# Optimization experiments

Hardware: AMD Instinct MI355X
Metric: run time of the kernel (lower is better)

## Reference

```python
import jax, jax.numpy as jnp
import numpy as np

N = 100000
E = 3200000
D = 128


def setup_inputs() -> dict:
    key = jax.random.key(0)
    k1, k2, k3, k4 = jax.random.split(key, 4)
    x = jax.random.normal(k1, (N, D), dtype=jnp.float32)
    edge_index = jax.random.randint(k2, (2, E), 0, N, dtype=jnp.int64)
    W1 = jax.random.normal(k3, (D, 16), dtype=jnp.float32) * (1.0 / np.sqrt(D))
    b1 = jnp.zeros((16,), dtype=jnp.float32)
    W2 = jax.random.normal(k4, (16, 2), dtype=jnp.float32) * (1.0 / np.sqrt(16))
    b2 = jnp.zeros((2,), dtype=jnp.float32)
    return {"x": x, "edge_index": edge_index, "W1": W1, "b1": b1, "W2": W2, "b2": b2}


def _gcn_conv(h, src, dst, norm, W, b):
    # transform first (out_dim <= in_dim), then normalized scatter-add aggregation
    h = h @ W                                   # [N, out]
    msg = h[src] * norm[:, None]                # [E+N, out] gathered messages
    agg = jax.ops.segment_sum(msg, dst, num_segments=N)
    return agg + b


def reference(x, edge_index, W1, b1, W2, b2):
    loops = jnp.arange(N, dtype=edge_index.dtype)
    src = jnp.concatenate([edge_index[0], loops])   # row (message source)
    dst = jnp.concatenate([edge_index[1], loops])   # col (aggregation target)
    # symmetric GCN normalization: deg over dst, norm = d^-1/2[src] * d^-1/2[dst]
    deg = jax.ops.segment_sum(jnp.ones_like(src, dtype=x.dtype), dst, num_segments=N)
    dinv = jnp.where(deg > 0, jax.lax.rsqrt(deg), 0.0)
    norm = dinv[src] * dinv[dst]

    h = _gcn_conv(x, src, dst, norm, W1, b1)
    h = jax.nn.relu(h)
    h = _gcn_conv(h, src, dst, norm, W2, b2)
    return jax.nn.log_softmax(h, axis=1)
```

## Files before the change

### kernel.cpp

```cpp
#include <hip/hip_runtime.h>
#include <hip/hip_fp16.h>
#include <math.h>

#define N_NODES 100000
#define N_EDGES 3200000
#define D_IN    128
#define H1      16

#define PSH     8
#define NPB     200
#define NB      500
#define CAP     9936
#define PBLK    512
#define CHUNK   6250
#define ELS_CAP 13760
#define NLINES  (ELS_CAP / 16)
#define CSTRIDE 32
#define MROWS   64
#define BITQ    5

__device__ __forceinline__ unsigned bkt(int d) {
    return (unsigned)(((unsigned long long)(unsigned)d * 671089ull) >> 27);
}


__global__ __launch_bounds__(512) void k_partition(const int* __restrict__ ei,
                                                   int* __restrict__ cursor,
                                                   unsigned int* __restrict__ eop) {
    __shared__ int h[512];
    __shared__ int loff[512];
    __shared__ int resv[NB];
    __shared__ int wsum[8], wpre[8];
    __shared__ unsigned short owner[NLINES];
    __shared__ unsigned char rank8[CHUNK];
    __shared__ unsigned int els[ELS_CAP];
    int t = threadIdx.x;
    h[t] = 0;
    __syncthreads();
    int c0 = blockIdx.x * CHUNK;
    const int2* s2 = (const int2*)(ei + c0);
    const int2* d2 = (const int2*)(ei + N_EDGES + c0);
    for (int i = t; i < CHUNK / 2; i += 512) {
        int2 dd = d2[i];
        rank8[2 * i]     = (unsigned char)atomicAdd(&h[bkt(dd.x)], 1);
        rank8[2 * i + 1] = (unsigned char)atomicAdd(&h[bkt(dd.y)], 1);
    }
    __syncthreads();
    int cp = (h[t] + 15) & ~15;
    int lane = t & 63, w = t >> 6;
    int v = cp;
#pragma unroll
    for (int o = 1; o < 64; o <<= 1) {
        int u = __shfl_up(v, o);
        if (lane >= o) v += u;
    }
    if (lane == 63) wsum[w] = v;
    __syncthreads();
    if (t < 8) {
        int s = wsum[t];
#pragma unroll
        for (int o = 1; o < 8; o <<= 1) {
            int u = __shfl_up(s, o);
            if (t >= o) s += u;
        }
        wpre[t] = s;
    }
    __syncthreads();
    int inc = v + ((w > 0) ? wpre[w - 1] : 0);
    int totalpad = wpre[7];
    int ex = inc - cp;
    loff[t] = ex;
    if (t < NB && cp) {
        resv[t] = atomicAdd(&cursor[t * CSTRIDE], cp);
        int l0 = ex >> 4;
        for (int k = 0; k < (cp >> 4); ++k) owner[l0 + k] = (unsigned short)t;
    }
    for (int i4 = t; i4 < (totalpad >> 2); i4 += 512)
        ((uint4*)els)[i4] = make_uint4(0xFFFFFFFFu, 0xFFFFFFFFu, 0xFFFFFFFFu, 0xFFFFFFFFu);
    __syncthreads();
    for (int i = t; i < CHUNK / 2; i += 512) {
        int2 ss = s2[i];
        int2 dd = d2[i];
        unsigned bx = bkt(dd.x), by = bkt(dd.y);
        els[loff[bx] + (int)rank8[2 * i]] =
            ((unsigned)ss.x << PSH) | (unsigned)(dd.x - (int)(bx * NPB));
        els[loff[by] + (int)rank8[2 * i + 1]] =
            ((unsigned)ss.y << PSH) | (unsigned)(dd.y - (int)(by * NPB));
    }
    __syncthreads();
    for (int i4 = t; i4 < (totalpad >> 2); i4 += 512) {
        int b   = owner[i4 >> 2];
        int pos = resv[b] + (4 * i4 - loff[b]);
        if (pos + 3 < CAP)
            *(uint4*)(eop + (size_t)b * CAP + pos) = ((const uint4*)els)[i4];
    }
}

__global__ __launch_bounds__(512) void k_build(const int* __restrict__ cursor,
                                               unsigned int* __restrict__ eop,
                                               int* __restrict__ nstart,
                                               int* __restrict__ ndeg,
                                               float* __restrict__ dinv) {
    __shared__ int cnt[256];
    __shared__ int off[256];
    __shared__ int wsum[4], wpre[4];
    int t = threadIdx.x, b = blockIdx.x;
    if (t < 256) cnt[t] = 0;
    __syncthreads();
    int n = cursor[b * CSTRIDE]; if (n > CAP) n = CAP;
    int nq = n >> 2;
    unsigned int* reg = eop + (size_t)b * CAP;
    uint4 st[BITQ];
#pragma unroll
    for (int it = 0; it < BITQ; ++it) {
        int i4 = t + it * 512;
        if (i4 < nq) {
            uint4 wv = ((const uint4*)reg)[i4];
            unsigned int e0 = wv.x, e1 = wv.y, e2 = wv.z, e3 = wv.w;
            int r;
            if ((int)e0 >= 0) { r = atomicAdd(&cnt[e0 & 0xFF], 1); e0 |= (unsigned)r << 25; }
            if ((int)e1 >= 0) { r = atomicAdd(&cnt[e1 & 0xFF], 1); e1 |= (unsigned)r << 25; }
            if ((int)e2 >= 0) { r = atomicAdd(&cnt[e2 & 0xFF], 1); e2 |= (unsigned)r << 25; }
            if ((int)e3 >= 0) { r = atomicAdd(&cnt[e3 & 0xFF], 1); e3 |= (unsigned)r << 25; }
            st[it] = make_uint4(e0, e1, e2, e3);
        }
    }
    __syncthreads();
    int lane = t & 63, w = t >> 6;
    int v = 0;
    if (t < 256) {
        v = cnt[t];
#pragma unroll
        for (int o = 1; o < 64; o <<= 1) {
            int u = __shfl_up(v, o);
            if (lane >= o) v += u;
        }
        if (lane == 63) wsum[w] = v;
    }
    __syncthreads();
    if (t < 4) {
        int s = wsum[t];
#pragma unroll
        for (int o = 1; o < 4; o <<= 1) {
            int u = __shfl_up(s, o);
            if (t >= o) s += u;
        }
        wpre[t] = s;
    }
    __syncthreads();
    if (t < 256) {
        int val = cnt[t];
        int ex = (v + ((w > 0) ? wpre[w - 1] : 0)) - val;
        off[t] = ex;
        if (t < NPB) {
            int node = b * NPB + t;
            nstart[node] = b * CAP + ex;
            ndeg[node]   = val;
            dinv[node]   = rsqrtf((float)(val + 1));
        }
    }
    __syncthreads();
#pragma unroll
    for (int it = 0; it < BITQ; ++it) {
        int i4 = t + it * 512;
        if (i4 < nq) {
            uint4 wv = st[it];
            unsigned int e; unsigned s;
            e = wv.x; s = (e >> PSH) & 0x1FFFFu;
            if (s < N_NODES) reg[off[e & 0xFF] + (int)((e >> 25) & 0x7F)] = s;
            e = wv.y; s = (e >> PSH) & 0x1FFFFu;
            if (s < N_NODES) reg[off[e & 0xFF] + (int)((e >> 25) & 0x7F)] = s;
            e = wv.z; s = (e >> PSH) & 0x1FFFFu;
            if (s < N_NODES) reg[off[e & 0xFF] + (int)((e >> 25) & 0x7F)] = s;
            e = wv.w; s = (e >> PSH) & 0x1FFFFu;
            if (s < N_NODES) reg[off[e & 0xFF] + (int)((e >> 25) & 0x7F)] = s;
        }
    }
}

__global__ __launch_bounds__(256) void k_mm1(const float* __restrict__ x,
                                             const float* __restrict__ W1,
                                             const float* __restrict__ dinv,
                                             __half* __restrict__ h1h) {
    __shared__ float sX[MROWS][D_IN + 1];
    int t = threadIdx.x;
    int r0 = blockIdx.x * MROWS;
    for (int i = t; i < MROWS * (D_IN / 4); i += 256) {
        int row = i >> 5, c4 = i & 31;
        int grow = r0 + row;
        float4 v = (grow < N_NODES) ? ((const float4*)x)[(size_t)grow * 32 + c4]
                                    : make_float4(0.f, 0.f, 0.f, 0.f);
        sX[row][c4 * 4 + 0] = v.x; sX[row][c4 * 4 + 1] = v.y;
        sX[row][c4 * 4 + 2] = v.z; sX[row][c4 * 4 + 3] = v.w;
    }
    __syncthreads();
    int lane = t & 63;
    int c0 = __builtin_amdgcn_readfirstlane((t >> 6) * 4);
    float a0 = 0.f, a1 = 0.f, a2 = 0.f, a3 = 0.f;
#pragma unroll 4
    for (int d = 0; d < D_IN; ++d) {
        float xv = sX[lane][d];
        a0 = fmaf(xv, W1[d * 16 + c0 + 0], a0);
        a1 = fmaf(xv, W1[d * 16 + c0 + 1], a1);
        a2 = fmaf(xv, W1[d * 16 + c0 + 2], a2);
        a3 = fmaf(xv, W1[d * 16 + c0 + 3], a3);
    }
    int grow = r0 + lane;
    if (grow < N_NODES) {
        float di = dinv[grow];
        __half2* o = (__half2*)(h1h + (size_t)grow * H1 + c0);
        o[0] = __floats2half2_rn(a0 * di, a1 * di);
        o[1] = __floats2half2_rn(a2 * di, a3 * di);
    }
}

__global__ __launch_bounds__(256) void k_agg1(const unsigned int* __restrict__ eop,
                                              const int* __restrict__ nstart,
                                              const int* __restrict__ ndeg,
                                              const __half* __restrict__ h1h,
                                              const float* __restrict__ dinv,
                                              const float* __restrict__ b1,
                                              const float* __restrict__ W2,
                                              float2* __restrict__ h2f) {
    int t = threadIdx.x;
    int g = t >> 3, l = t & 7;
    int base = (t & 63) & ~7;
    int node = blockIdx.x * 32 + g;
    int e0 = nstart[node], deg = ndeg[node];
    const __half2* H = (const __half2*)h1h;
    float a0 = 0.f, a1 = 0.f, c0 = 0.f, c1 = 0.f;
    int nfull = deg & ~7;
    int jend = e0 + nfull;
    int s_cur = (nfull > 0) ? (int)eop[e0 + l] : 0;
    for (int j = e0; j < jend; j += 8) {
        int s_nxt = (j + 8 < jend) ? (int)eop[j + 8 + l] : 0;
#pragma unroll
        for (int k = 0; k < 8; k += 2) {
            int sk0 = __shfl(s_cur, base + k);
            int sk1 = __shfl(s_cur, base + k + 1);
            float2 f0 = __half22float2(H[sk0 * 8 + l]);
            float2 f1 = __half22float2(H[sk1 * 8 + l]);
            a0 += f0.x; a1 += f0.y;
            c0 += f1.x; c1 += f1.y;
        }
        s_cur = s_nxt;
    }
    int r = deg - nfull;
    if (r) {
        int s = (l < r) ? (int)eop[jend + l] : -1;
#pragma unroll
        for (int k = 0; k < 8; ++k) {
            int sk = __shfl(s, base + k);
            int su = (sk >= 0) ? sk : 0;
            float m = (sk >= 0) ? 1.f : 0.f;
            float2 f = __half22float2(H[su * 8 + l]);
            a0 = fmaf(f.x, m, a0); a1 = fmaf(f.y, m, a1);
        }
    }
    float di = dinv[node];
    float2 self = __half22float2(H[node * 8 + l]);
    float s0 = (a0 + c0) + self.x, s1 = (a1 + c1) + self.y;
    float2 bb = ((const float2*)b1)[l];
    float h0 = fmaxf(fmaf(di, s0, bb.x), 0.f);
    float h1v = fmaxf(fmaf(di, s1, bb.y), 0.f);
    float4 wv = ((const float4*)W2)[l];
    float p0 = h0 * wv.x + h1v * wv.z;
    float p1 = h0 * wv.y + h1v * wv.w;
#pragma unroll
    for (int off = 1; off < 8; off <<= 1) {
        p0 += __shfl_xor(p0, off);
        p1 += __shfl_xor(p1, off);
    }
    if (l == 0) h2f[node] = make_float2(p0 * di, p1 * di);
}

__global__ __launch_bounds__(256) void k_agg2(const unsigned int* __restrict__ eop,
                                              const int* __restrict__ nstart,
                                              const int* __restrict__ ndeg,
                                              const float2* __restrict__ h2f,
                                              const float* __restrict__ dinv,
                                              const float* __restrict__ b2,
                                              float* __restrict__ out) {
    int tg = blockIdx.x * 256 + threadIdx.x;
    int node = tg >> 3, l = tg & 7;
    int e0 = nstart[node], e1 = e0 + ndeg[node];
    float ax = 0.f, ay = 0.f;
    int j = e0 + l;
    int sj = (j < e1) ? (int)eop[j] : 0;
    for (; j < e1; j += 8) {
        int sn = (j + 8 < e1) ? (int)eop[j + 8] : 0;
        float2 m = h2f[sj];
        ax += m.x; ay += m.y;
        sj = sn;
    }
    ax += __shfl_xor(ax, 1); ay += __shfl_xor(ay, 1);
    ax += __shfl_xor(ax, 2); ay += __shfl_xor(ay, 2);
    ax += __shfl_xor(ax, 4); ay += __shfl_xor(ay, 4);
    if (l == 0) {
        float di = dinv[node];
        float2 self = h2f[node];
        float a0 = fmaf(di, ax + self.x, b2[0]);
        float a1 = fmaf(di, ay + self.y, b2[1]);
        float m  = fmaxf(a0, a1);
        float lg = logf(expf(a0 - m) + expf(a1 - m));
        out[2 * node]     = a0 - m - lg;
        out[2 * node + 1] = a1 - m - lg;
    }
}

extern "C" void kernel_launch(void* const* d_in, const int* in_sizes, int n_in,
                              void* d_out, int out_size, void* d_ws, size_t ws_size,
                              hipStream_t stream) {
    const float* x  = (const float*)d_in[0];
    const int*   ei = (const int*)d_in[1];
    const float* W1 = (const float*)d_in[2];
    const float* b1 = (const float*)d_in[3];
    const float* W2 = (const float*)d_in[4];
    const float* b2 = (const float*)d_in[5];
    float* out = (float*)d_out;

    int*          cursor = (int*)d_ws;
    int*          nstart = cursor + 16384;
    int*          ndeg   = nstart + 100352;
    float*        dinv   = (float*)(ndeg + 100352);
    __half*       h1h    = (__half*)(dinv + 100352);
    float2*       h2f    = (float2*)(h1h + (size_t)100352 * H1);
    unsigned int* eop    = (unsigned int*)(h2f + 100352);

    hipMemsetAsync(cursor, 0, 16384 * sizeof(int), stream);

    k_partition<<<PBLK, 512, 0, stream>>>(ei, cursor, eop);
    k_build    <<<NB,   512, 0, stream>>>(cursor, eop, nstart, ndeg, dinv);
    k_mm1      <<<(N_NODES + MROWS - 1) / MROWS, 256, 0, stream>>>(x, W1, dinv, h1h);
    k_agg1     <<<N_NODES / 32, 256, 0, stream>>>(eop, nstart, ndeg, h1h, dinv, b1, W2, h2f);
    k_agg2     <<<N_NODES / 32, 256, 0, stream>>>(eop, nstart, ndeg, h2f, dinv, b2, out);
}
```

Before: 199.9 us.

## Keep partition entries in registers and stage LDS scatter in two halves

The partition kernel now loads src/dst once, computes the packed entry and bucket/rank in registers, and drops the rank8 shared array and the second global read of edges. The shared staging buffer is halved and the scatter/flush runs in two passes over halves of the padded range, cutting LDS per block to allow higher occupancy. This costs extra registers per thread and doubles the scatter loop work and barriers.

Result: no change. 199.8 us (-0.0%).

```diff
diff --git a/kernel.cpp b/kernel.cpp
--- a/kernel.cpp
+++ b/kernel.cpp
@@ -14,10 +14,12 @@
 #define PBLK    512
 #define CHUNK   6250
 #define ELS_CAP 13760
+#define ELS_H   6880
 #define NLINES  (ELS_CAP / 16)
 #define CSTRIDE 32
 #define MROWS   64
 #define BITQ    5
+#define IT2     7
 
 __device__ __forceinline__ unsigned bkt(int d) {
     return (unsigned)(((unsigned long long)(unsigned)d * 671089ull) >> 27);
@@ -32,18 +34,28 @@
     __shared__ int resv[NB];
     __shared__ int wsum[8], wpre[8];
     __shared__ unsigned short owner[NLINES];
-    __shared__ unsigned char rank8[CHUNK];
-    __shared__ unsigned int els[ELS_CAP];
+    __shared__ unsigned int els[ELS_H];
     int t = threadIdx.x;
     h[t] = 0;
     __syncthreads();
     int c0 = blockIdx.x * CHUNK;
     const int2* s2 = (const int2*)(ei + c0);
     const int2* d2 = (const int2*)(ei + N_EDGES + c0);
-    for (int i = t; i < CHUNK / 2; i += 512) {
-        int2 dd = d2[i];
-        rank8[2 * i]     = (unsigned char)atomicAdd(&h[bkt(dd.x)], 1);
-        rank8[2 * i + 1] = (unsigned char)atomicAdd(&h[bkt(dd.y)], 1);
+    unsigned ent0[IT2], ent1[IT2], br0[IT2], br1[IT2];
+#pragma unroll
+    for (int it = 0; it < IT2; ++it) {
+        int i2 = t + it * 512;
+        if (i2 < CHUNK / 2) {
+            int2 ss = s2[i2];
+            int2 dd = d2[i2];
+            unsigned bx = bkt(dd.x), by = bkt(dd.y);
+            unsigned rx = (unsigned)atomicAdd(&h[bx], 1);
+            unsigned ry = (unsigned)atomicAdd(&h[by], 1);
+            ent0[it] = ((unsigned)ss.x << PSH) | (unsigned)(dd.x - (int)(bx * NPB));
+            ent1[it] = ((unsigned)ss.y << PSH) | (unsigned)(dd.y - (int)(by * NPB));
+            br0[it]  = (bx << 8) | rx;
+            br1[it]  = (by << 8) | ry;
+        }
     }
     __syncthreads();
     int cp = (h[t] + 15) & ~15;
@@ -75,24 +87,33 @@
         int l0 = ex >> 4;
         for (int k = 0; k < (cp >> 4); ++k) owner[l0 + k] = (unsigned short)t;
     }
-    for (int i4 = t; i4 < (totalpad >> 2); i4 += 512)
-        ((uint4*)els)[i4] = make_uint4(0xFFFFFFFFu, 0xFFFFFFFFu, 0xFFFFFFFFu, 0xFFFFFFFFu);
-    __syncthreads();
-    for (int i = t; i < CHUNK / 2; i += 512) {
-        int2 ss = s2[i];
-        int2 dd = d2[i];
-        unsigned bx = bkt(dd.x), by = bkt(dd.y);
-        els[loff[bx] + (int)rank8[2 * i]] =
-            ((unsigned)ss.x << PSH) | (unsigned)(dd.x - (int)(bx * NPB));
-        els[loff[by] + (int)rank8[2 * i + 1]] =
-            ((unsigned)ss.y << PSH) | (unsigned)(dd.y - (int)(by * NPB));
-    }
-    __syncthreads();
-    for (int i4 = t; i4 < (totalpad >> 2); i4 += 512) {
-        int b   = owner[i4 >> 2];
-        int pos = resv[b] + (4 * i4 - loff[b]);
-        if (pos + 3 < CAP)
-            *(uint4*)(eop + (size_t)b * CAP + pos) = ((const uint4*)els)[i4];
+    for (int half = 0; half < 2; ++half) {
+        int base = half * ELS_H;
+        int hi = (totalpad < base + ELS_H) ? totalpad : base + ELS_H;
+        int cnt4 = (hi - base) >> 2;
+        for (int i4 = t; i4 < cnt4; i4 += 512)
+            ((uint4*)els)[i4] = make_uint4(0xFFFFFFFFu, 0xFFFFFFFFu,
+                                           0xFFFFFFFFu, 0xFFFFFFFFu);
+        __syncthreads();
+#pragma unroll
+        for (int it = 0; it < IT2; ++it) {
+            int i2 = t + it * 512;
+            if (i2 < CHUNK / 2) {
+                int p0 = loff[br0[it] >> 8] + (int)(br0[it] & 0xFF);
+                if (p0 >= base && p0 < hi) els[p0 - base] = ent0[it];
+                int p1 = loff[br1[it] >> 8] + (int)(br1[it] & 0xFF);
+                if (p1 >= base && p1 < hi) els[p1 - base] = ent1[it];
+            }
+        }
+        __syncthreads();
+        for (int i4 = t; i4 < cnt4; i4 += 512) {
+            int gi = base + 4 * i4;
+            int b   = owner[gi >> 4];
+            int pos = resv[b] + (gi - loff[b]);
+            if (pos + 3 < CAP)
+                *(uint4*)(eop + (size_t)b * CAP + pos) = ((const uint4*)els)[i4];
+        }
+        __syncthreads();
     }
 }
 
```
